# Kernel optimization log

Hardware: AMD Instinct MI355X
Metric: run time of the kernel (lower is better)

The kernel has to match this reference:

```python
import jax, jax.numpy as jnp
import numpy as np

H = 8
HID = 512
DH = HID // H
EPS = 1e-5


def _ln(x, g, b):
    mu = jnp.mean(x, axis=-1, keepdims=True)
    var = jnp.mean(jnp.square(x - mu), axis=-1, keepdims=True)
    return (x - mu) * jax.lax.rsqrt(var + EPS) * g + b


def setup_inputs() -> dict:
    key = jax.random.key(0)
    ks = jax.random.split(key, 40)
    L, M, P, D = 4096, 1024, 4096, 512

    def xav(k, shp):
        lim = np.sqrt(6.0 / (shp[0] + shp[1]))
        return jax.random.uniform(k, shp, jnp.float32, -lim, lim)

    inp = {
        'lncRNA_embedding': jax.random.normal(ks[0], (L, D), jnp.float32),
        'miRNA_embedding': jax.random.normal(ks[1], (M, D), jnp.float32),
        'protein_embedding': jax.random.normal(ks[2], (P, D), jnp.float32),
        'lncRNA_miRNA_matrix': jax.random.randint(ks[3], (L, M), 0, 2, jnp.int32),
        'protein_miRNA_matrix': jax.random.randint(ks[4], (P, M), 0, 2, jnp.int32),
    }
    names = ['Wl', 'Wm', 'Wp', 'Wql', 'Wkl', 'Wvl', 'Wqp', 'Wkp', 'Wvp']
    for i, n in enumerate(names):
        inp[n] = xav(ks[5 + i], (HID, HID))
        inp['b' + n[1:]] = jnp.zeros((HID,), jnp.float32)
    inp['Wml'] = xav(ks[20], (2 * HID, D // 2))
    inp['bml'] = jnp.zeros((D // 2,), jnp.float32)
    inp['Wmp'] = xav(ks[21], (2 * HID, D // 2))
    inp['bmp'] = jnp.zeros((D // 2,), jnp.float32)
    inp['g1'] = jnp.ones((D // 2,), jnp.float32)
    inp['be1'] = jnp.zeros((D // 2,), jnp.float32)
    inp['g2'] = jnp.ones((D // 2,), jnp.float32)
    inp['be2'] = jnp.zeros((D // 2,), jnp.float32)
    # first three linears take dim-D input (D == HID here)
    return inp


def reference(lncRNA_embedding, miRNA_embedding, protein_embedding,
              lncRNA_miRNA_matrix, protein_miRNA_matrix,
              Wl, bl, Wm, bm, Wp, bp,
              Wql, bql, Wkl, bkl, Wvl, bvl,
              Wqp, bqp, Wkp, bkp, Wvp, bvp,
              Wml, bml, Wmp, bmp, g1, be1, g2, be2):
    L = lncRNA_embedding.shape[0]
    M = miRNA_embedding.shape[0]
    P = protein_embedding.shape[0]

    lt = lncRNA_embedding @ Wl + bl          # [L, HID]
    mt = miRNA_embedding @ Wm + bm           # [M, HID]
    pt = protein_embedding @ Wp + bp         # [P, HID]

    def heads(x, W, b, n):
        return (x @ W + b).reshape(n, H, DH)

    Ql = heads(lt, Wql, bql, L)              # [L, H, DH]
    Kl = heads(mt, Wkl, bkl, M)
    Vl = heads(mt, Wvl, bvl, M)
    Qp = heads(pt, Wqp, bqp, P)
    Kp = heads(mt, Wkp, bkp, M)
    Vp = heads(mt, Wvp, bvp, M)

    scale = 1.0 / np.sqrt(DH)
    sl = jnp.einsum('lhd,mhd->hlm', Ql, Kl) * scale      # [H, L, M]
    sl = jnp.where(lncRNA_miRNA_matrix[None] == 0, -1e9, sl)
    awl = jax.nn.softmax(sl, axis=-1)

    sp = jnp.einsum('phd,mhd->hpm', Qp, Kp) * scale      # [H, P, M]
    sp = jnp.where(protein_miRNA_matrix[None] == 0, -1e9, sp)
    awp = jax.nn.softmax(sp, axis=-1)

    ctx_l = jax.nn.relu(jnp.einsum('hlm,mhd->lhd', awl, Vl).reshape(L, HID))
    ctx_p = jax.nn.relu(jnp.einsum('hpm,mhd->phd', awp, Vp).reshape(P, HID))

    mutual = jnp.einsum('hlm,hpm->lp', awl, awp) / H     # [L, P]

    fin_l = ctx_l + mutual @ ctx_p
    fin_p = ctx_p + mutual.T @ ctx_l

    out_l = _ln(jnp.concatenate([lt, fin_l], axis=-1) @ Wml + bml, g1, be1)
    out_p = _ln(jnp.concatenate([fin_p, pt], axis=-1) @ Wmp + bmp, g2, be2)
    return out_l, out_p
```

## Files before the change

kernel.cpp:

```cpp
#include <hip/hip_runtime.h>
#include <hip/hip_bf16.h>

using bf16 = __hip_bfloat16;
typedef __attribute__((ext_vector_type(8))) short short8;
typedef __attribute__((ext_vector_type(4))) float floatx4;
typedef __attribute__((ext_vector_type(8))) unsigned short ushort8;
typedef __attribute__((ext_vector_type(4))) int i32x4;
typedef __attribute__((ext_vector_type(8))) int i32x8;

__device__ __forceinline__ float b2f(unsigned short u) {
    union { unsigned int i; float f; } x; x.i = ((unsigned int)u) << 16; return x.f;
}

__device__ __forceinline__ void async16(const void* g, void* l) {
    __builtin_amdgcn_global_load_lds((const __attribute__((address_space(1))) void*)g,
                                     (__attribute__((address_space(3))) void*)l,
                                     16, 0, 0);
}

__device__ __forceinline__ unsigned char f2e4m3(float f) {
    unsigned s = (__float_as_uint(f) >> 24) & 0x80u;
    f = fminf(fabsf(f), 448.f);
    if (f < 0.015625f) {
        int d = (int)rintf(f * 512.f);
        return (unsigned char)(s | (unsigned)d);
    }
    int E = (int)((__float_as_uint(f) >> 23) & 255u) - 127;
    float ulp_inv = __uint_as_float((unsigned)(127 + 3 - E) << 23);
    int m = (int)rintf(f * ulp_inv);
    int n = (m == 16) ? ((E + 8) << 3) : (((E + 7) << 3) + (m - 8));
    if (n > 0x7E) n = 0x7E;
    return (unsigned char)(s | (unsigned)n);
}

__global__ void sniff_dtype(const unsigned short* p, int* flag) {
    int wild = 0;
    for (int i = threadIdx.x; i < 256; i += 64) {
        float a = fabsf(b2f(p[i]));
        if (!(a <= 1e4f)) wild++;
    }
#pragma unroll
    for (int o = 1; o < 64; o <<= 1) wild += __shfl_xor(wild, o);
    if (threadIdx.x == 0) *flag = (wild > 16) ? 1 : 0;
}

struct Cvt { const void* src; bf16* dst; int n; };
struct CvtTable { Cvt e[18]; };

__global__ __launch_bounds__(256) void convert_inputs(CvtTable t, const int* flag) {
    const Cvt c = t.e[blockIdx.y];
    const bool f32 = (*flag != 0);
    const int stride = gridDim.x * 256 * 8;
    for (int i = (blockIdx.x * 256 + threadIdx.x) * 8; i < c.n; i += stride) {
        if (f32) {
            const float* s = (const float*)c.src + i;
#pragma unroll
            for (int j = 0; j < 8; ++j) c.dst[i + j] = __float2bfloat16(s[j]);
        } else {
            *(ushort8*)((unsigned short*)c.dst + i) =
                *(const ushort8*)((const unsigned short*)c.src + i);
        }
    }
}

struct TT9 { const void* src[9]; bf16* dst[9]; };

__global__ __launch_bounds__(256) void transpose_sq9(TT9 t, const int* flag) {
    __shared__ bf16 tile[32][33];
    const void* in = t.src[blockIdx.z];
    bf16* out = t.dst[blockIdx.z];
    const bool f32 = (*flag != 0);
    const int tx = threadIdx.x & 31;
    const int ty = threadIdx.x >> 5;
    const int bc = blockIdx.x * 32;
    const int br = blockIdx.y * 32;
#pragma unroll
    for (int i = 0; i < 32; i += 8) {
        const size_t idx = (size_t)(br + ty + i) * 512 + bc + tx;
        tile[ty + i][tx] = f32 ? __float2bfloat16(((const float*)in)[idx])
                               : ((const bf16*)in)[idx];
    }
    __syncthreads();
#pragma unroll
    for (int i = 0; i < 32; i += 8)
        out[(size_t)(bc + ty + i) * 512 + br + tx] = tile[tx][ty + i];
}

struct TaPair { const void* in[2]; bf16* out[2]; };

__global__ __launch_bounds__(256) void transpose_any_pair(
    TaPair P, int ils, int R, int C, const int* __restrict__ flag)
{
    __shared__ bf16 tile[32][33];
    const void* in = P.in[blockIdx.z];
    bf16* out = P.out[blockIdx.z];
    const bool f32 = (*flag != 0);
    const int tx = threadIdx.x & 31;
    const int ty = threadIdx.x >> 5;
    const int bc = blockIdx.x * 32;
    const int br = blockIdx.y * 32;
#pragma unroll
    for (int i = 0; i < 32; i += 8) {
        const size_t idx = (size_t)(br + ty + i) * ils + bc + tx;
        tile[ty + i][tx] = f32 ? __float2bfloat16(((const float*)in)[idx])
                               : ((const bf16*)in)[idx];
    }
    __syncthreads();
#pragma unroll
    for (int i = 0; i < 32; i += 8)
        out[(size_t)(bc + ty + i) * R + br + tx] = tile[tx][ty + i];
}

struct TqPair { const bf16* in[2]; unsigned char* out[2]; };

__global__ __launch_bounds__(256) void transpose_q8_pair(
    TqPair P, int ils, int R, int C, float vs)
{
    __shared__ float tile[32][33];
    const bf16* in = P.in[blockIdx.z];
    unsigned char* out = P.out[blockIdx.z];
    const int tx = threadIdx.x & 31;
    const int ty = threadIdx.x >> 5;
    const int bc = blockIdx.x * 32;
    const int br = blockIdx.y * 32;
#pragma unroll
    for (int i = 0; i < 32; i += 8)
        tile[ty + i][tx] =
            __bfloat162float(in[(size_t)(br + ty + i) * ils + bc + tx]) * vs;
    __syncthreads();
#pragma unroll
    for (int i = 0; i < 32; i += 8)
        out[(size_t)(bc + ty + i) * R + br + tx] = f2e4m3(tile[tx][ty + i]);
}

__global__ __launch_bounds__(256) void transpose_b8(
    const unsigned char* __restrict__ in, unsigned char* __restrict__ out,
    int R, int C)
{
    __align__(16) __shared__ unsigned char tile[64][80];
    const int t  = threadIdx.x;
    const int r  = t & 63;
    const int cq = t >> 6;
    const int br = blockIdx.y * 64;
    const int bc = blockIdx.x * 64;
    *(i32x4*)&tile[r][cq * 16] =
        *(const i32x4*)(in + (size_t)(br + r) * C + bc + cq * 16);
    __syncthreads();
    unsigned char v[16];
#pragma unroll
    for (int j = 0; j < 16; ++j) v[j] = tile[cq * 16 + j][r];
    *(i32x4*)(out + (size_t)(bc + r) * R + br + cq * 16) = *(i32x4*)v;
}

struct BtArgs { const bf16* A; const bf16* B; void* C; const bf16* bias; };
struct BtPair { BtArgs s[2]; };

template <int BM, int BN, bool BIAS, bool F32OUT>
__global__ __launch_bounds__(256) void gemm_bt(
    BtPair P, int lda, int ldb, int ldc, int K, float scale)
{
    constexpr int WM = BM / 2;
    constexpr int WN = BN / 2;
    constexpr int TM = WM / 16;
    constexpr int TN = WN / 16;

    __align__(16) __shared__ bf16 As[BM * 64];
    __align__(16) __shared__ bf16 Bs[BN * 64];

    const BtArgs g = P.s[blockIdx.z];
    const int lane = threadIdx.x & 63;
    const int wv   = threadIdx.x >> 6;
    const int m_base = blockIdx.y * BM;
    const int n_base = blockIdx.x * BN;
    const int wm0 = (wv >> 1) * WM;
    const int wn0 = (wv & 1) * WN;

    floatx4 zero = {0.f, 0.f, 0.f, 0.f};
    floatx4 acc[TM][TN];
#pragma unroll
    for (int mt = 0; mt < TM; ++mt)
#pragma unroll
        for (int nt = 0; nt < TN; ++nt) acc[mt][nt] = zero;

    const int sr  = lane >> 3;
    const int sce = ((lane & 7) ^ sr) * 8;
    const int fr  = lane & 15;
    const int q   = lane >> 4;
    const int sw  = fr & 7;

    for (int k0 = 0; k0 < K; k0 += 64) {
#pragma unroll
        for (int cc = 0; cc < BM / 32; ++cc) {
            const int r0t = (wv + cc * 4) * 8;
            async16(g.A + (size_t)(m_base + r0t + sr) * lda + k0 + sce, &As[r0t * 64]);
        }
#pragma unroll
        for (int cc = 0; cc < BN / 32; ++cc) {
            const int r0t = (wv + cc * 4) * 8;
            async16(g.B + (size_t)(n_base + r0t + sr) * ldb + k0 + sce, &Bs[r0t * 64]);
        }
        __syncthreads();

#pragma unroll
        for (int s = 0; s < 2; ++s) {
            const int off = ((s * 4 + q) ^ sw) * 8;
            short8 af[TM], bfr[TN];
#pragma unroll
            for (int mt = 0; mt < TM; ++mt)
                af[mt] = *(const short8*)&As[(wm0 + mt * 16 + fr) * 64 + off];
#pragma unroll
            for (int nt = 0; nt < TN; ++nt)
                bfr[nt] = *(const short8*)&Bs[(wn0 + nt * 16 + fr) * 64 + off];
#pragma unroll
            for (int mt = 0; mt < TM; ++mt)
#pragma unroll
                for (int nt = 0; nt < TN; ++nt)
                    acc[mt][nt] = __builtin_amdgcn_mfma_f32_16x16x32_bf16(
                        af[mt], bfr[nt], acc[mt][nt], 0, 0, 0);
        }
        __syncthreads();
    }

    const int er = lane >> 4;
    const int ec = lane & 15;
#pragma unroll
    for (int nt = 0; nt < TN; ++nt) {
        const int col = n_base + wn0 + nt * 16 + ec;
        float bv = 0.f;
        if constexpr (BIAS) bv = __bfloat162float(g.bias[col]);
#pragma unroll
        for (int mt = 0; mt < TM; ++mt) {
#pragma unroll
            for (int r = 0; r < 4; ++r) {
                const int row = m_base + wm0 + mt * 16 + er * 4 + r;
                float v = acc[mt][nt][r] * scale + bv;
                if constexpr (F32OUT)
                    ((float*)g.C)[(size_t)row * ldc + col] = v;
                else
                    ((bf16*)g.C)[(size_t)row * ldc + col] = __float2bfloat16(v);
            }
        }
    }
}

struct SegTab { const bf16* W[3]; const bf16* bias[3]; bf16* C[3]; int ldc[3]; int rs[3]; };

__global__ __launch_bounds__(256) void gemm_bt_seg(
    const bf16* __restrict__ A, SegTab T, int K)
{
    constexpr int BM = 64, BN = 64, TM = 2, TN = 2;
    __align__(16) __shared__ bf16 As[BM * 64];
    __align__(16) __shared__ bf16 Bs[BN * 64];

    const int lane = threadIdx.x & 63;
    const int wv   = threadIdx.x >> 6;
    const int gm   = blockIdx.y * BM;
    const int seg  = (gm >= 5120) ? 2 : ((gm >= 4096) ? 1 : 0);
    const bf16* B  = T.W[seg];
    const bf16* bias = T.bias[seg];
    bf16* C        = T.C[seg];
    const int ldc  = T.ldc[seg];
    const int m_base = gm - T.rs[seg];
    const int n_base = blockIdx.x * BN;
    const int wm0 = (wv >> 1) * 32;
    const int wn0 = (wv & 1) * 32;

    floatx4 zero = {0.f, 0.f, 0.f, 0.f};
    floatx4 acc[TM][TN];
#pragma unroll
    for (int mt = 0; mt < TM; ++mt)
#pragma unroll
        for (int nt = 0; nt < TN; ++nt) acc[mt][nt] = zero;

    const int sr  = lane >> 3;
    const int sce = ((lane & 7) ^ sr) * 8;
    const int fr  = lane & 15;
    const int q   = lane >> 4;
    const int sw  = fr & 7;

    for (int k0 = 0; k0 < K; k0 += 64) {
#pragma unroll
        for (int cc = 0; cc < 2; ++cc) {
            const int r0t = (wv + cc * 4) * 8;
            async16(A + (size_t)(gm + r0t + sr) * 512 + k0 + sce, &As[r0t * 64]);
            async16(B + (size_t)(n_base + r0t + sr) * 512 + k0 + sce, &Bs[r0t * 64]);
        }
        __syncthreads();
#pragma unroll
        for (int s = 0; s < 2; ++s) {
            const int off = ((s * 4 + q) ^ sw) * 8;
            short8 af[TM], bfr[TN];
#pragma unroll
            for (int mt = 0; mt < TM; ++mt)
                af[mt] = *(const short8*)&As[(wm0 + mt * 16 + fr) * 64 + off];
#pragma unroll
            for (int nt = 0; nt < TN; ++nt)
                bfr[nt] = *(const short8*)&Bs[(wn0 + nt * 16 + fr) * 64 + off];
#pragma unroll
            for (int mt = 0; mt < TM; ++mt)
#pragma unroll
                for (int nt = 0; nt < TN; ++nt)
                    acc[mt][nt] = __builtin_amdgcn_mfma_f32_16x16x32_bf16(
                        af[mt], bfr[nt], acc[mt][nt], 0, 0, 0);
        }
        __syncthreads();
    }

    const int er = lane >> 4;
    const int ec = lane & 15;
#pragma unroll
    for (int nt = 0; nt < TN; ++nt) {
        const int col = n_base + wn0 + nt * 16 + ec;
        const float bv = __bfloat162float(bias[col]);
#pragma unroll
        for (int mt = 0; mt < TM; ++mt) {
#pragma unroll
            for (int r = 0; r < 4; ++r) {
                const int row = m_base + wm0 + mt * 16 + er * 4 + r;
                C[(size_t)row * ldc + col] =
                    __float2bfloat16(acc[mt][nt][r] + bv);
            }
        }
    }
}

struct B8Args { const unsigned char* A; const unsigned char* B; bf16* C; };
struct B8Pair { B8Args s[2]; };

template <int BM, int BN, bool RELU>
__global__ __launch_bounds__(256) void gemm_bt8(
    B8Pair P, int lda, long long a_kshift, int ldb, int ldc, int K, float scale)
{
    constexpr int WM = BM / 2;
    constexpr int WN = BN / 2;
    constexpr int TM = WM / 16;
    constexpr int TN = WN / 16;

    __align__(16) __shared__ unsigned char As[BM * 64];
    __align__(16) __shared__ unsigned char Bs[BN * 64];

    const B8Args g = P.s[blockIdx.z];
    const int lane = threadIdx.x & 63;
    const int wv   = threadIdx.x >> 6;
    const int m_base = blockIdx.y * BM;
    const int n_base = blockIdx.x * BN;
    const unsigned char* A = g.A + (long long)blockIdx.x * a_kshift;

    const int wm0 = (wv >> 1) * WM;
    const int wn0 = (wv & 1) * WN;

    floatx4 zero = {0.f, 0.f, 0.f, 0.f};
    floatx4 acc[TM][TN];
#pragma unroll
    for (int mt = 0; mt < TM; ++mt)
#pragma unroll
        for (int nt = 0; nt < TN; ++nt) acc[mt][nt] = zero;

    const int ar = lane >> 2;
    const int ac = (((lane & 3) ^ (ar & 3)) * 16);
    const int fr = lane & 15;
    const int q  = lane >> 4;
    const int sw = fr & 3;

    for (int k0 = 0; k0 < K; k0 += 64) {
#pragma unroll
        for (int cc = 0; cc < BM / 16; cc += 4) {
            const int r0t = (wv + cc) * 16;
            async16(A + (size_t)(m_base + r0t + ar) * lda + k0 + ac, &As[r0t * 64]);
        }
#pragma unroll
        for (int cc = 0; cc < BN / 16; cc += 4) {
            const int r0t = (wv + cc) * 16;
            async16(g.B + (size_t)(n_base + r0t + ar) * ldb + k0 + ac, &Bs[r0t * 64]);
        }
        __syncthreads();

#pragma unroll
        for (int s = 0; s < 2; ++s) {
            const int boff = (((s * 2 + (q >> 1)) ^ sw) * 16) + (q & 1) * 8;
            long af[TM], bfr[TN];
#pragma unroll
            for (int mt = 0; mt < TM; ++mt)
                af[mt] = *(const long*)&As[(wm0 + mt * 16 + fr) * 64 + boff];
#pragma unroll
            for (int nt = 0; nt < TN; ++nt)
                bfr[nt] = *(const long*)&Bs[(wn0 + nt * 16 + fr) * 64 + boff];
#pragma unroll
            for (int mt = 0; mt < TM; ++mt)
#pragma unroll
                for (int nt = 0; nt < TN; ++nt)
                    acc[mt][nt] = __builtin_amdgcn_mfma_f32_16x16x32_fp8_fp8(
                        af[mt], bfr[nt], acc[mt][nt], 0, 0, 0);
        }
        __syncthreads();
    }

    const int er = lane >> 4;
    const int ec = lane & 15;
#pragma unroll
    for (int nt = 0; nt < TN; ++nt) {
        const int col = n_base + wn0 + nt * 16 + ec;
#pragma unroll
        for (int mt = 0; mt < TM; ++mt) {
#pragma unroll
            for (int r = 0; r < 4; ++r) {
                const int row = m_base + wm0 + mt * 16 + er * 4 + r;
                float v = acc[mt][nt][r] * scale;
                if constexpr (RELU) v = fmaxf(v, 0.f);
                g.C[(size_t)row * ldc + col] = __float2bfloat16(v);
            }
        }
    }
}

struct MxArgs { const unsigned char* A; const unsigned char* B; void* C; const bf16* Cz; };
struct MxPair { MxArgs s[2]; };

template <int BM, int BN, bool ADDC0, bool FP8OUT>
__global__ __launch_bounds__(256) void gemm_bt8mx(
    MxPair P, int lda, int ldb, int ldc, int ldc0, int K, float scale)
{
    constexpr int WM = BM / 2;
    constexpr int WN = BN / 2;
    constexpr int TM = WM / 16;
    constexpr int TN = WN / 16;

    __align__(16) __shared__ unsigned char As[BM * 128];
    __align__(16) __shared__ unsigned char Bs[BN * 128];

    const MxArgs g = P.s[blockIdx.z];
    const int lane = threadIdx.x & 63;
    const int wv   = threadIdx.x >> 6;
    const int m_base = blockIdx.y * BM;
    const int n_base = blockIdx.x * BN;

    const int wm0 = (wv >> 1) * WM;
    const int wn0 = (wv & 1) * WN;

    floatx4 zero = {0.f, 0.f, 0.f, 0.f};
    floatx4 acc[TM][TN];
#pragma unroll
    for (int mt = 0; mt < TM; ++mt)
#pragma unroll
        for (int nt = 0; nt < TN; ++nt) acc[mt][nt] = zero;

    const int sr = lane >> 3;
    const int sc = ((lane & 7) ^ sr) * 16;
    const int fr = lane & 15;
    const int q  = lane >> 4;
    const int sw = fr & 7;

    for (int k0 = 0; k0 < K; k0 += 128) {
#pragma unroll
        for (int cc = 0; cc < BM / 32; ++cc) {
            const int r0t = (wv + cc * 4) * 8;
            async16(g.A + (size_t)(m_base + r0t + sr) * lda + k0 + sc, &As[r0t * 128]);
        }
#pragma unroll
        for (int cc = 0; cc < BN / 32; ++cc) {
            const int r0t = (wv + cc * 4) * 8;
            async16(g.B + (size_t)(n_base + r0t + sr) * ldb + k0 + sc, &Bs[r0t * 128]);
        }
        __syncthreads();

        i32x8 af[TM], bf8[TN];
#pragma unroll
        for (int mt = 0; mt < TM; ++mt) {
            const unsigned char* rp = &As[(wm0 + mt * 16 + fr) * 128];
            i32x4 lo = *(const i32x4*)(rp + (((q * 2 + 0) ^ sw) * 16));
            i32x4 hi = *(const i32x4*)(rp + (((q * 2 + 1) ^ sw) * 16));
            af[mt] = __builtin_shufflevector(lo, hi, 0, 1, 2, 3, 4, 5, 6, 7);
        }
#pragma unroll
        for (int nt = 0; nt < TN; ++nt) {
            const unsigned char* rp = &Bs[(wn0 + nt * 16 + fr) * 128];
            i32x4 lo = *(const i32x4*)(rp + (((q * 2 + 0) ^ sw) * 16));
            i32x4 hi = *(const i32x4*)(rp + (((q * 2 + 1) ^ sw) * 16));
            bf8[nt] = __builtin_shufflevector(lo, hi, 0, 1, 2, 3, 4, 5, 6, 7);
        }
#pragma unroll
        for (int mt = 0; mt < TM; ++mt)
#pragma unroll
            for (int nt = 0; nt < TN; ++nt)
                acc[mt][nt] = __builtin_amdgcn_mfma_scale_f32_16x16x128_f8f6f4(
                    af[mt], bf8[nt], acc[mt][nt],
                    0, 0, 0, 127, 0, 127);
        __syncthreads();
    }

    const int er = lane >> 4;
    const int ec = lane & 15;
#pragma unroll
    for (int nt = 0; nt < TN; ++nt) {
        const int col = n_base + wn0 + nt * 16 + ec;
#pragma unroll
        for (int mt = 0; mt < TM; ++mt) {
#pragma unroll
            for (int r = 0; r < 4; ++r) {
                const int row = m_base + wm0 + mt * 16 + er * 4 + r;
                float v = acc[mt][nt][r] * scale;
                if constexpr (ADDC0) v += __bfloat162float(g.Cz[(size_t)row * ldc0 + col]);
                if constexpr (FP8OUT)
                    ((unsigned char*)g.C)[(size_t)row * ldc + col] = f2e4m3(v);
                else
                    ((bf16*)g.C)[(size_t)row * ldc + col] = __float2bfloat16(v);
            }
        }
    }
}

struct ScArgs { const bf16* Q; const bf16* K; const int* mask; unsigned char* aw; };
struct ScPair { ScArgs s[2]; };

__global__ __launch_bounds__(256) void scores_mfma(
    ScPair P, int ldk, float scale)
{
    __shared__ float wred[16][4];
    __shared__ float wsum[16][4];

    const ScArgs g = P.s[blockIdx.z];
    const int t    = threadIdx.x;
    const int lane = t & 63;
    const int w    = t >> 6;
    const int h    = blockIdx.y;
    const int r0   = blockIdx.x * 16;
    const int fr   = lane & 15;
    const int fq   = lane >> 4;
    const int cbase = w * 256;

    const short* Qs = (const short*)g.Q + (size_t)(r0 + fr) * 512 + h * 64 + fq * 8;
    short8 a0 = *(const short8*)(Qs);
    short8 a1 = *(const short8*)(Qs + 32);

    floatx4 accs[16];
    const short* Kb = (const short*)g.K + h * 64 + fq * 8;
#pragma unroll
    for (int c = 0; c < 16; ++c) {
        const int krow = cbase + c * 16 + fr;
        short8 b0 = *(const short8*)(Kb + (size_t)krow * ldk);
        short8 b1 = *(const short8*)(Kb + (size_t)krow * ldk + 32);
        floatx4 acc = {0.f, 0.f, 0.f, 0.f};
        acc = __builtin_amdgcn_mfma_f32_16x16x32_bf16(a0, b0, acc, 0, 0, 0);
        acc = __builtin_amdgcn_mfma_f32_16x16x32_bf16(a1, b1, acc, 0, 0, 0);
        accs[c] = acc;
    }

    float mxr[4] = {-3e38f, -3e38f, -3e38f, -3e38f};
#pragma unroll
    for (int c = 0; c < 16; ++c) {
        const int col = cbase + c * 16 + fr;
#pragma unroll
        for (int r = 0; r < 4; ++r) {
            const int row = r0 + fq * 4 + r;
            float v = (g.mask[(size_t)row * 1024 + col] == 0) ? -1e9f
                                                              : accs[c][r] * scale;
            accs[c][r] = v;
            mxr[r] = fmaxf(mxr[r], v);
        }
    }
#pragma unroll
    for (int o = 1; o < 16; o <<= 1)
#pragma unroll
        for (int r = 0; r < 4; ++r) mxr[r] = fmaxf(mxr[r], __shfl_xor(mxr[r], o));
    if (fr == 0)
#pragma unroll
        for (int r = 0; r < 4; ++r) wred[fq * 4 + r][w] = mxr[r];
    __syncthreads();

    float mx[4], sm[4] = {0.f, 0.f, 0.f, 0.f};
#pragma unroll
    for (int r = 0; r < 4; ++r) {
        const int row = fq * 4 + r;
        mx[r] = fmaxf(fmaxf(wred[row][0], wred[row][1]),
                      fmaxf(wred[row][2], wred[row][3]));
    }
#pragma unroll
    for (int c = 0; c < 16; ++c)
#pragma unroll
        for (int r = 0; r < 4; ++r) {
            float e = __expf(accs[c][r] - mx[r]);
            accs[c][r] = e;
            sm[r] += e;
        }
#pragma unroll
    for (int o = 1; o < 16; o <<= 1)
#pragma unroll
        for (int r = 0; r < 4; ++r) sm[r] += __shfl_xor(sm[r], o);
    if (fr == 0)
#pragma unroll
        for (int r = 0; r < 4; ++r) wsum[fq * 4 + r][w] = sm[r];
    __syncthreads();

    float inv[4];
#pragma unroll
    for (int r = 0; r < 4; ++r) {
        const int row = fq * 4 + r;
        inv[r] = 32.0f / (wsum[row][0] + wsum[row][1] + wsum[row][2] + wsum[row][3]);
    }
#pragma unroll
    for (int c = 0; c < 16; ++c) {
        const int col = cbase + c * 16 + fr;
#pragma unroll
        for (int r = 0; r < 4; ++r) {
            const int row = r0 + fq * 4 + r;
            g.aw[(size_t)row * 8192 + h * 1024 + col] = f2e4m3(accs[c][r] * inv[r]);
        }
    }
}

__global__ __launch_bounds__(256) void ln_all(
    const float* __restrict__ X,
    const bf16* __restrict__ g1, const bf16* __restrict__ be1,
    const bf16* __restrict__ g2, const bf16* __restrict__ be2,
    void* __restrict__ out, const int* __restrict__ flag)
{
    const bool f32 = (*flag != 0);
    const int lane = threadIdx.x & 63;
    const int wv   = threadIdx.x >> 6;
    const int row  = blockIdx.x * 4 + wv;
    const bf16* gg = (row >= 4096) ? g2 : g1;
    const bf16* bb = (row >= 4096) ? be2 : be1;
    const float* x = X + (size_t)row * 256;
    float v[4], s = 0.f, s2 = 0.f;
#pragma unroll
    for (int i = 0; i < 4; ++i) {
        v[i] = x[lane + 64 * i];
        s += v[i]; s2 += v[i] * v[i];
    }
#pragma unroll
    for (int o = 1; o < 64; o <<= 1) { s += __shfl_xor(s, o); s2 += __shfl_xor(s2, o); }
    const float mu  = s * (1.0f / 256.0f);
    const float var = fmaxf(s2 * (1.0f / 256.0f) - mu * mu, 0.0f);
    const float inv = rsqrtf(var + 1e-5f);
#pragma unroll
    for (int i = 0; i < 4; ++i) {
        const int c = lane + 64 * i;
        const float y = (v[i] - mu) * inv * __bfloat162float(gg[c]) + __bfloat162float(bb[c]);
        if (f32) ((float*)out)[(size_t)row * 256 + c] = y;
        else     ((bf16*)out)[(size_t)row * 256 + c] = __float2bfloat16(y);
    }
}

extern "C" void kernel_launch(void* const* d_in, const int* in_sizes, int n_in,
                              void* d_out, int out_size, void* d_ws, size_t ws_size,
                              hipStream_t stream)
{
    const int L = 4096, Mm = 1024, P = 4096;

    const int* mask_l = (const int*)d_in[3];
    const int* mask_p = (const int*)d_in[4];

    char* ws = (char*)d_ws;
    size_t off = 0;
    auto alloc = [&](size_t bytes) {
        void* p = ws + off; off += (bytes + 255) & ~(size_t)255; return p;
    };

    int*  flag   = (int*)alloc(256);
    bf16* wt_all = (bf16*)alloc((size_t)9 * 512 * 512 * 2);
    bf16* WmlT   = (bf16*)alloc(1024 * 256 * 2);
    bf16* WmpT   = (bf16*)alloc(1024 * 256 * 2);
    bf16* b_l    = (bf16*)alloc(512 * 2);
    bf16* b_m    = (bf16*)alloc(512 * 2);
    bf16* b_p    = (bf16*)alloc(512 * 2);
    bf16* b_ql   = (bf16*)alloc(512 * 2);
    bf16* b_qp   = (bf16*)alloc(512 * 2);
    bf16* bcat   = (bf16*)alloc(2048 * 2);
    bf16* bml_c  = (bf16*)alloc(256 * 2);
    bf16* bmp_c  = (bf16*)alloc(256 * 2);
    bf16* g1c    = (bf16*)alloc(256 * 2);
    bf16* be1c   = (bf16*)alloc(256 * 2);
    bf16* g2c    = (bf16*)alloc(256 * 2);
    bf16* be2c   = (bf16*)alloc(256 * 2);
    bf16* emb_all = (bf16*)alloc((size_t)(L + Mm + P) * 512 * 2);
    bf16* embl   = emb_all;
    bf16* embm   = emb_all + (size_t)L * 512;
    bf16* embp   = embm + (size_t)Mm * 512;
    bf16* cat_l  = (bf16*)alloc((size_t)L * 1024 * 2);
    bf16* cat_p  = (bf16*)alloc((size_t)P * 1024 * 2);
    bf16* mt     = (bf16*)alloc((size_t)Mm * 512 * 2);
    bf16* Ql     = (bf16*)alloc((size_t)L * 512 * 2);
    bf16* Qp     = (bf16*)alloc((size_t)P * 512 * 2);
    bf16* kvcat  = (bf16*)alloc((size_t)Mm * 2048 * 2);
    unsigned char* V8lT = (unsigned char*)alloc((size_t)512 * Mm);
    unsigned char* V8pT = (unsigned char*)alloc((size_t)512 * Mm);
    bf16* ctx_l  = (bf16*)alloc((size_t)L * 512 * 2);
    bf16* ctx_p  = (bf16*)alloc((size_t)P * 512 * 2);
    unsigned char* ctx8lT = (unsigned char*)alloc((size_t)512 * L);
    unsigned char* ctx8pT = (unsigned char*)alloc((size_t)512 * P);
    unsigned char* mutual8 = (unsigned char*)alloc((size_t)L * P);
    unsigned char* awl8 = (unsigned char*)alloc((size_t)L * 8192);
    unsigned char* awp8 = (unsigned char*)alloc((size_t)P * 8192);
    unsigned char* mutual8T = awl8;
    float* tmp1 = (float*)awp8;

    sniff_dtype<<<1, 64, 0, stream>>>((const unsigned short*)d_in[0], flag);

    CvtTable tab;
    tab.e[0]  = { d_in[0],  embl, L * 512 };
    tab.e[1]  = { d_in[1],  embm, Mm * 512 };
    tab.e[2]  = { d_in[2],  embp, P * 512 };
    tab.e[3]  = { d_in[6],  b_l,  512 };
    tab.e[4]  = { d_in[8],  b_m,  512 };
    tab.e[5]  = { d_in[10], b_p,  512 };
    tab.e[6]  = { d_in[12], b_ql, 512 };
    tab.e[7]  = { d_in[18], b_qp, 512 };
    tab.e[8]  = { d_in[14], bcat,        512 };
    tab.e[9]  = { d_in[16], bcat + 512,  512 };
    tab.e[10] = { d_in[20], bcat + 1024, 512 };
    tab.e[11] = { d_in[22], bcat + 1536, 512 };
    tab.e[12] = { d_in[24], bml_c, 256 };
    tab.e[13] = { d_in[26], bmp_c, 256 };
    tab.e[14] = { d_in[27], g1c,  256 };
    tab.e[15] = { d_in[28], be1c, 256 };
    tab.e[16] = { d_in[29], g2c,  256 };
    tab.e[17] = { d_in[30], be2c, 256 };
    convert_inputs<<<dim3(256, 18), 256, 0, stream>>>(tab, flag);

    TT9 tt;
    const int slot_of[9] = {0, 1, 2, 3, 5, 6, 4, 7, 8};
    for (int i = 0; i < 9; ++i) {
        tt.src[i] = d_in[5 + 2 * i];
        tt.dst[i] = wt_all + (size_t)slot_of[i] * 512 * 512;
    }
    transpose_sq9<<<dim3(16, 16, 9), 256, 0, stream>>>(tt, flag);
    TaPair tw = { { d_in[23], d_in[25] }, { WmlT, WmpT } };
    transpose_any_pair<<<dim3(8, 32, 2), 256, 0, stream>>>(tw, 256, 1024, 256, flag);

    bf16* WlT  = wt_all;
    bf16* WmT  = wt_all + (size_t)1 * 512 * 512;
    bf16* WpT  = wt_all + (size_t)2 * 512 * 512;
    bf16* WqlT = wt_all + (size_t)3 * 512 * 512;
    bf16* WqpT = wt_all + (size_t)4 * 512 * 512;
    bf16* WkvT = wt_all + (size_t)5 * 512 * 512;

    SegTab st;
    st.W[0] = WlT;  st.bias[0] = b_l; st.C[0] = cat_l;       st.ldc[0] = 1024; st.rs[0] = 0;
    st.W[1] = WmT;  st.bias[1] = b_m; st.C[1] = mt;          st.ldc[1] = 512;  st.rs[1] = 4096;
    st.W[2] = WpT;  st.bias[2] = b_p; st.C[2] = cat_p + 512; st.ldc[2] = 1024; st.rs[2] = 5120;
    gemm_bt_seg<<<dim3(8, 144), 256, 0, stream>>>(emb_all, st, 512);

    BtPair qp = { { { cat_l,       WqlT, Ql, b_ql },
                    { cat_p + 512, WqpT, Qp, b_qp } } };
    gemm_bt<64, 64, true, false><<<dim3(8, 64, 2), 256, 0, stream>>>(
        qp, 1024, 512, 512, 512, 1.0f);
    BtPair kv = { { { mt, WkvT, kvcat, bcat }, { mt, WkvT, kvcat, bcat } } };
    gemm_bt<64, 64, true, false><<<dim3(32, 16, 1), 256, 0, stream>>>(
        kv, 512, 512, 2048, 512, 1.0f);

    TqPair v8 = { { kvcat + 512, kvcat + 1536 }, { V8lT, V8pT } };
    transpose_q8_pair<<<dim3(16, 32, 2), 256, 0, stream>>>(v8, 2048, 1024, 512, 4.0f);

    ScPair sc = { { { Ql, kvcat,        mask_l, awl8 },
                    { Qp, kvcat + 1024, mask_p, awp8 } } };
    scores_mfma<<<dim3(256, 8, 2), 256, 0, stream>>>(sc, 2048, 0.125f);

    B8Pair cx = { { { awl8, V8lT, ctx_l }, { awp8, V8pT, ctx_p } } };
    gemm_bt8<64, 64, true><<<dim3(8, 64, 2), 256, 0, stream>>>(
        cx, 8192, 1024, 1024, 512, 1024, 1.0f / 128.0f);

    TqPair c8 = { { ctx_l, ctx_p }, { ctx8lT, ctx8pT } };
    transpose_q8_pair<<<dim3(16, 128, 2), 256, 0, stream>>>(c8, 512, 4096, 512, 16.0f);

    MxPair mu = { { { awl8, awp8, mutual8, nullptr },
                    { awl8, awp8, mutual8, nullptr } } };
    gemm_bt8mx<128, 128, false, true><<<dim3(32, 32, 1), 256, 0, stream>>>(
        mu, 8192, 8192, 4096, 0, 8192, 0.03125f);
    transpose_b8<<<dim3(64, 64), 256, 0, stream>>>(mutual8, mutual8T, 4096, 4096);

    MxPair fn = { { { mutual8,  ctx8pT, cat_l + 512, ctx_l },
                    { mutual8T, ctx8lT, cat_p,       ctx_p } } };
    gemm_bt8mx<64, 64, true, false><<<dim3(8, 64, 2), 256, 0, stream>>>(
        fn, 4096, 4096, 1024, 512, 4096, 1.0f / 4096.0f);

    BtPair fp = { { { cat_l, WmlT, tmp1,                    bml_c },
                    { cat_p, WmpT, tmp1 + (size_t)L * 256,  bmp_c } } };
    gemm_bt<64, 64, true, true><<<dim3(4, 64, 2), 256, 0, stream>>>(
        fp, 1024, 1024, 256, 1024, 1.0f);

    ln_all<<<dim3(2048), 256, 0, stream>>>(tmp1, g1c, be1c, g2c, be2c, d_out, flag);
}
```

Measured before the change: 563.9 us.

## Fuse prep kernels, merge Q/KV GEMMs, fuse transposes into producer epilogues

Merges dtype sniffing, input conversion and weight transposes into a single prep kernel that sniffs the dtype per wave. The Q and KV projections now run in one launch. The V fp8 transpose is folded into the scores kernel, and the ctx fp8 transpose into the ctx GEMM epilogue. The mutual GEMM writes its transposed copy directly in its epilogue, uses larger tiles, and gets its own buffer instead of aliasing awl8. This is meant to cut launch count and extra memory passes, at the cost of more complex kernels and some redundant sniff work in every block.

```diff
diff --git a/kernel.cpp b/kernel.cpp
--- a/kernel.cpp
+++ b/kernel.cpp
@@ -33,213 +33,80 @@
     return (unsigned char)(s | (unsigned)n);
 }
 
-__global__ void sniff_dtype(const unsigned short* p, int* flag) {
+__device__ __forceinline__ bool sniff_wave(const unsigned short* p) {
+    const int lane = threadIdx.x & 63;
     int wild = 0;
-    for (int i = threadIdx.x; i < 256; i += 64) {
-        float a = fabsf(b2f(p[i]));
-        if (!(a <= 1e4f)) wild++;
+#pragma unroll
+    for (int j = 0; j < 4; ++j) {
+        float a = fabsf(b2f(p[lane * 4 + j]));
+        wild += !(a <= 1e4f);
     }
 #pragma unroll
     for (int o = 1; o < 64; o <<= 1) wild += __shfl_xor(wild, o);
-    if (threadIdx.x == 0) *flag = (wild > 16) ? 1 : 0;
+    return wild > 16;
 }
 
 struct Cvt { const void* src; bf16* dst; int n; };
-struct CvtTable { Cvt e[18]; };
-
-__global__ __launch_bounds__(256) void convert_inputs(CvtTable t, const int* flag) {
-    const Cvt c = t.e[blockIdx.y];
-    const bool f32 = (*flag != 0);
-    const int stride = gridDim.x * 256 * 8;
-    for (int i = (blockIdx.x * 256 + threadIdx.x) * 8; i < c.n; i += stride) {
-        if (f32) {
-            const float* s = (const float*)c.src + i;
-#pragma unroll
-            for (int j = 0; j < 8; ++j) c.dst[i + j] = __float2bfloat16(s[j]);
-        } else {
-            *(ushort8*)((unsigned short*)c.dst + i) =
-                *(const ushort8*)((const unsigned short*)c.src + i);
-        }
-    }
-}
-
-struct TT9 { const void* src[9]; bf16* dst[9]; };
-
-__global__ __launch_bounds__(256) void transpose_sq9(TT9 t, const int* flag) {
+struct PrepArgs {
+    Cvt cv[18];
+    const void* tsrc[11];
+    bf16* tdst[11];
+    const unsigned short* sn;
+};
+
+__global__ __launch_bounds__(256) void prep(PrepArgs a) {
+    const bool f32 = sniff_wave(a.sn);
+    const int y = blockIdx.y;
     __shared__ bf16 tile[32][33];
-    const void* in = t.src[blockIdx.z];
-    bf16* out = t.dst[blockIdx.z];
-    const bool f32 = (*flag != 0);
+
+    if (y < 18) {
+        const Cvt c = a.cv[y];
+        const int stride = gridDim.x * 256 * 8;
+        for (int i = (blockIdx.x * 256 + threadIdx.x) * 8; i < c.n; i += stride) {
+            if (f32) {
+                const float* s = (const float*)c.src + i;
+#pragma unroll
+                for (int j = 0; j < 8; ++j) c.dst[i + j] = __float2bfloat16(s[j]);
+            } else {
+                *(ushort8*)((unsigned short*)c.dst + i) =
+                    *(const ushort8*)((const unsigned short*)c.src + i);
+            }
+        }
+        return;
+    }
+
     const int tx = threadIdx.x & 31;
     const int ty = threadIdx.x >> 5;
-    const int bc = blockIdx.x * 32;
-    const int br = blockIdx.y * 32;
-#pragma unroll
-    for (int i = 0; i < 32; i += 8) {
-        const size_t idx = (size_t)(br + ty + i) * 512 + bc + tx;
-        tile[ty + i][tx] = f32 ? __float2bfloat16(((const float*)in)[idx])
-                               : ((const bf16*)in)[idx];
-    }
-    __syncthreads();
-#pragma unroll
-    for (int i = 0; i < 32; i += 8)
-        out[(size_t)(bc + ty + i) * 512 + br + tx] = tile[tx][ty + i];
-}
-
-struct TaPair { const void* in[2]; bf16* out[2]; };
-
-__global__ __launch_bounds__(256) void transpose_any_pair(
-    TaPair P, int ils, int R, int C, const int* __restrict__ flag)
-{
-    __shared__ bf16 tile[32][33];
-    const void* in = P.in[blockIdx.z];
-    bf16* out = P.out[blockIdx.z];
-    const bool f32 = (*flag != 0);
-    const int tx = threadIdx.x & 31;
-    const int ty = threadIdx.x >> 5;
-    const int bc = blockIdx.x * 32;
-    const int br = blockIdx.y * 32;
-#pragma unroll
-    for (int i = 0; i < 32; i += 8) {
-        const size_t idx = (size_t)(br + ty + i) * ils + bc + tx;
-        tile[ty + i][tx] = f32 ? __float2bfloat16(((const float*)in)[idx])
-                               : ((const bf16*)in)[idx];
-    }
-    __syncthreads();
-#pragma unroll
-    for (int i = 0; i < 32; i += 8)
-        out[(size_t)(bc + ty + i) * R + br + tx] = tile[tx][ty + i];
-}
-
-struct TqPair { const bf16* in[2]; unsigned char* out[2]; };
-
-__global__ __launch_bounds__(256) void transpose_q8_pair(
-    TqPair P, int ils, int R, int C, float vs)
-{
-    __shared__ float tile[32][33];
-    const bf16* in = P.in[blockIdx.z];
-    unsigned char* out = P.out[blockIdx.z];
-    const int tx = threadIdx.x & 31;
-    const int ty = threadIdx.x >> 5;
-    const int bc = blockIdx.x * 32;
-    const int br = blockIdx.y * 32;
-#pragma unroll
-    for (int i = 0; i < 32; i += 8)
-        tile[ty + i][tx] =
-            __bfloat162float(in[(size_t)(br + ty + i) * ils + bc + tx]) * vs;
-    __syncthreads();
-#pragma unroll
-    for (int i = 0; i < 32; i += 8)
-        out[(size_t)(bc + ty + i) * R + br + tx] = f2e4m3(tile[tx][ty + i]);
-}
-
-__global__ __launch_bounds__(256) void transpose_b8(
-    const unsigned char* __restrict__ in, unsigned char* __restrict__ out,
-    int R, int C)
-{
-    __align__(16) __shared__ unsigned char tile[64][80];
-    const int t  = threadIdx.x;
-    const int r  = t & 63;
-    const int cq = t >> 6;
-    const int br = blockIdx.y * 64;
-    const int bc = blockIdx.x * 64;
-    *(i32x4*)&tile[r][cq * 16] =
-        *(const i32x4*)(in + (size_t)(br + r) * C + bc + cq * 16);
-    __syncthreads();
-    unsigned char v[16];
-#pragma unroll
-    for (int j = 0; j < 16; ++j) v[j] = tile[cq * 16 + j][r];
-    *(i32x4*)(out + (size_t)(bc + r) * R + br + cq * 16) = *(i32x4*)v;
-}
-
-struct BtArgs { const bf16* A; const bf16* B; void* C; const bf16* bias; };
-struct BtPair { BtArgs s[2]; };
-
-template <int BM, int BN, bool BIAS, bool F32OUT>
-__global__ __launch_bounds__(256) void gemm_bt(
-    BtPair P, int lda, int ldb, int ldc, int K, float scale)
-{
-    constexpr int WM = BM / 2;
-    constexpr int WN = BN / 2;
-    constexpr int TM = WM / 16;
-    constexpr int TN = WN / 16;
-
-    __align__(16) __shared__ bf16 As[BM * 64];
-    __align__(16) __shared__ bf16 Bs[BN * 64];
-
-    const BtArgs g = P.s[blockIdx.z];
-    const int lane = threadIdx.x & 63;
-    const int wv   = threadIdx.x >> 6;
-    const int m_base = blockIdx.y * BM;
-    const int n_base = blockIdx.x * BN;
-    const int wm0 = (wv >> 1) * WM;
-    const int wn0 = (wv & 1) * WN;
-
-    floatx4 zero = {0.f, 0.f, 0.f, 0.f};
-    floatx4 acc[TM][TN];
-#pragma unroll
-    for (int mt = 0; mt < TM; ++mt)
-#pragma unroll
-        for (int nt = 0; nt < TN; ++nt) acc[mt][nt] = zero;
-
-    const int sr  = lane >> 3;
-    const int sce = ((lane & 7) ^ sr) * 8;
-    const int fr  = lane & 15;
-    const int q   = lane >> 4;
-    const int sw  = fr & 7;
-
-    for (int k0 = 0; k0 < K; k0 += 64) {
-#pragma unroll
-        for (int cc = 0; cc < BM / 32; ++cc) {
-            const int r0t = (wv + cc * 4) * 8;
-            async16(g.A + (size_t)(m_base + r0t + sr) * lda + k0 + sce, &As[r0t * 64]);
-        }
-#pragma unroll
-        for (int cc = 0; cc < BN / 32; ++cc) {
-            const int r0t = (wv + cc * 4) * 8;
-            async16(g.B + (size_t)(n_base + r0t + sr) * ldb + k0 + sce, &Bs[r0t * 64]);
-        }
-        __syncthreads();
-
-#pragma unroll
-        for (int s = 0; s < 2; ++s) {
-            const int off = ((s * 4 + q) ^ sw) * 8;
-            short8 af[TM], bfr[TN];
-#pragma unroll
-            for (int mt = 0; mt < TM; ++mt)
-                af[mt] = *(const short8*)&As[(wm0 + mt * 16 + fr) * 64 + off];
-#pragma unroll
-            for (int nt = 0; nt < TN; ++nt)
-                bfr[nt] = *(const short8*)&Bs[(wn0 + nt * 16 + fr) * 64 + off];
-#pragma unroll
-            for (int mt = 0; mt < TM; ++mt)
-#pragma unroll
-                for (int nt = 0; nt < TN; ++nt)
-                    acc[mt][nt] = __builtin_amdgcn_mfma_f32_16x16x32_bf16(
-                        af[mt], bfr[nt], acc[mt][nt], 0, 0, 0);
-        }
-        __syncthreads();
-    }
-
-    const int er = lane >> 4;
-    const int ec = lane & 15;
-#pragma unroll
-    for (int nt = 0; nt < TN; ++nt) {
-        const int col = n_base + wn0 + nt * 16 + ec;
-        float bv = 0.f;
-        if constexpr (BIAS) bv = __bfloat162float(g.bias[col]);
-#pragma unroll
-        for (int mt = 0; mt < TM; ++mt) {
-#pragma unroll
-            for (int r = 0; r < 4; ++r) {
-                const int row = m_base + wm0 + mt * 16 + er * 4 + r;
-                float v = acc[mt][nt][r] * scale + bv;
-                if constexpr (F32OUT)
-                    ((float*)g.C)[(size_t)row * ldc + col] = v;
-                else
-                    ((bf16*)g.C)[(size_t)row * ldc + col] = __float2bfloat16(v);
-            }
-        }
+    if (y < 27) {
+        const void* in = a.tsrc[y - 18];
+        bf16* out = a.tdst[y - 18];
+        const int bc = (blockIdx.x & 15) * 32;
+        const int br = (blockIdx.x >> 4) * 32;
+#pragma unroll
+        for (int i = 0; i < 32; i += 8) {
+            const size_t idx = (size_t)(br + ty + i) * 512 + bc + tx;
+            tile[ty + i][tx] = f32 ? __float2bfloat16(((const float*)in)[idx])
+                                   : ((const bf16*)in)[idx];
+        }
+        __syncthreads();
+#pragma unroll
+        for (int i = 0; i < 32; i += 8)
+            out[(size_t)(bc + ty + i) * 512 + br + tx] = tile[tx][ty + i];
+    } else {
+        const void* in = a.tsrc[y - 27 + 9];
+        bf16* out = a.tdst[y - 27 + 9];
+        const int bc = (blockIdx.x & 7) * 32;
+        const int br = (blockIdx.x >> 3) * 32;
+#pragma unroll
+        for (int i = 0; i < 32; i += 8) {
+            const size_t idx = (size_t)(br + ty + i) * 256 + bc + tx;
+            tile[ty + i][tx] = f32 ? __float2bfloat16(((const float*)in)[idx])
+                                   : ((const bf16*)in)[idx];
+        }
+        __syncthreads();
+#pragma unroll
+        for (int i = 0; i < 32; i += 8)
+            out[(size_t)(bc + ty + i) * 1024 + br + tx] = tile[tx][ty + i];
     }
 }
 
@@ -248,20 +115,20 @@
 __global__ __launch_bounds__(256) void gemm_bt_seg(
     const bf16* __restrict__ A, SegTab T, int K)
 {
-    constexpr int BM = 64, BN = 64, TM = 2, TN = 2;
-    __align__(16) __shared__ bf16 As[BM * 64];
-    __align__(16) __shared__ bf16 Bs[BN * 64];
+    constexpr int TM = 2, TN = 2;
+    __align__(16) __shared__ bf16 As[64 * 64];
+    __align__(16) __shared__ bf16 Bs[64 * 64];
 
     const int lane = threadIdx.x & 63;
     const int wv   = threadIdx.x >> 6;
-    const int gm   = blockIdx.y * BM;
+    const int gm   = blockIdx.y * 64;
     const int seg  = (gm >= 5120) ? 2 : ((gm >= 4096) ? 1 : 0);
     const bf16* B  = T.W[seg];
     const bf16* bias = T.bias[seg];
     bf16* C        = T.C[seg];
     const int ldc  = T.ldc[seg];
     const int m_base = gm - T.rs[seg];
-    const int n_base = blockIdx.x * BN;
+    const int n_base = blockIdx.x * 64;
     const int wm0 = (wv >> 1) * 32;
     const int wn0 = (wv & 1) * 32;
 
@@ -313,41 +180,38 @@
         const int col = n_base + wn0 + nt * 16 + ec;
         const float bv = __bfloat162float(bias[col]);
 #pragma unroll
-        for (int mt = 0; mt < TM; ++mt) {
+        for (int mt = 0; mt < TM; ++mt)
 #pragma unroll
             for (int r = 0; r < 4; ++r) {
                 const int row = m_base + wm0 + mt * 16 + er * 4 + r;
-                C[(size_t)row * ldc + col] =
-                    __float2bfloat16(acc[mt][nt][r] + bv);
+                C[(size_t)row * ldc + col] = __float2bfloat16(acc[mt][nt][r] + bv);
             }
-        }
-    }
-}
-
-struct B8Args { const unsigned char* A; const unsigned char* B; bf16* C; };
-struct B8Pair { B8Args s[2]; };
-
-template <int BM, int BN, bool RELU>
-__global__ __launch_bounds__(256) void gemm_bt8(
-    B8Pair P, int lda, long long a_kshift, int ldb, int ldc, int K, float scale)
+    }
+}
+
+struct BtArgs { const bf16* A; const bf16* B; void* C; const bf16* bias;
+                int lda, ldb, ldc; };
+struct BtSet { BtArgs s[3]; };
+
+template <bool F32OUT, bool REMAP2>
+__global__ __launch_bounds__(256) void gemm_btx(BtSet P, int K, float scale)
 {
-    constexpr int WM = BM / 2;
-    constexpr int WN = BN / 2;
-    constexpr int TM = WM / 16;
-    constexpr int TN = WN / 16;
-
-    __align__(16) __shared__ unsigned char As[BM * 64];
-    __align__(16) __shared__ unsigned char Bs[BN * 64];
-
-    const B8Args g = P.s[blockIdx.z];
+    constexpr int TM = 2, TN = 2;
+    __align__(16) __shared__ bf16 As[64 * 64];
+    __align__(16) __shared__ bf16 Bs[64 * 64];
+
+    const BtArgs g = P.s[blockIdx.z];
+    int bx = blockIdx.x, by = blockIdx.y;
+    if (REMAP2 && blockIdx.z == 2) {
+        const int flat = by * gridDim.x + bx;
+        bx = flat & 31; by = flat >> 5;
+    }
     const int lane = threadIdx.x & 63;
     const int wv   = threadIdx.x >> 6;
-    const int m_base = blockIdx.y * BM;
-    const int n_base = blockIdx.x * BN;
-    const unsigned char* A = g.A + (long long)blockIdx.x * a_kshift;
-
-    const int wm0 = (wv >> 1) * WM;
-    const int wn0 = (wv & 1) * WN;
+    const int m_base = by * 64;
+    const int n_base = bx * 64;
+    const int wm0 = (wv >> 1) * 32;
+    const int wn0 = (wv & 1) * 32;
 
     floatx4 zero = {0.f, 0.f, 0.f, 0.f};
     floatx4 acc[TM][TN];
@@ -356,40 +220,35 @@
 #pragma unroll
         for (int nt = 0; nt < TN; ++nt) acc[mt][nt] = zero;
 
-    const int ar = lane >> 2;
-    const int ac = (((lane & 3) ^ (ar & 3)) * 16);
-    const int fr = lane & 15;
-    const int q  = lane >> 4;
-    const int sw = fr & 3;
+    const int sr  = lane >> 3;
+    const int sce = ((lane & 7) ^ sr) * 8;
+    const int fr  = lane & 15;
+    const int q   = lane >> 4;
+    const int sw  = fr & 7;
 
     for (int k0 = 0; k0 < K; k0 += 64) {
 #pragma unroll
-        for (int cc = 0; cc < BM / 16; cc += 4) {
-            const int r0t = (wv + cc) * 16;
-            async16(A + (size_t)(m_base + r0t + ar) * lda + k0 + ac, &As[r0t * 64]);
-        }
-#pragma unroll
-        for (int cc = 0; cc < BN / 16; cc += 4) {
-            const int r0t = (wv + cc) * 16;
-            async16(g.B + (size_t)(n_base + r0t + ar) * ldb + k0 + ac, &Bs[r0t * 64]);
-        }
-        __syncthreads();
-
+        for (int cc = 0; cc < 2; ++cc) {
+            const int r0t = (wv + cc * 4) * 8;
+            async16(g.A + (size_t)(m_base + r0t + sr) * g.lda + k0 + sce, &As[r0t * 64]);
+            async16(g.B + (size_t)(n_base + r0t + sr) * g.ldb + k0 + sce, &Bs[r0t * 64]);
+        }
+        __syncthreads();
 #pragma unroll
         for (int s = 0; s < 2; ++s) {
-            const int boff = (((s * 2 + (q >> 1)) ^ sw) * 16) + (q & 1) * 8;
-            long af[TM], bfr[TN];
+            const int off = ((s * 4 + q) ^ sw) * 8;
+            short8 af[TM], bfr[TN];
 #pragma unroll
             for (int mt = 0; mt < TM; ++mt)
-                af[mt] = *(const long*)&As[(wm0 + mt * 16 + fr) * 64 + boff];
+                af[mt] = *(const short8*)&As[(wm0 + mt * 16 + fr) * 64 + off];
 #pragma unroll
             for (int nt = 0; nt < TN; ++nt)
-                bfr[nt] = *(const long*)&Bs[(wn0 + nt * 16 + fr) * 64 + boff];
+                bfr[nt] = *(const short8*)&Bs[(wn0 + nt * 16 + fr) * 64 + off];
 #pragma unroll
             for (int mt = 0; mt < TM; ++mt)
 #pragma unroll
                 for (int nt = 0; nt < TN; ++nt)
-                    acc[mt][nt] = __builtin_amdgcn_mfma_f32_16x16x32_fp8_fp8(
+                    acc[mt][nt] = __builtin_amdgcn_mfma_f32_16x16x32_bf16(
                         af[mt], bfr[nt], acc[mt][nt], 0, 0, 0);
         }
         __syncthreads();
@@ -400,123 +259,51 @@
 #pragma unroll
     for (int nt = 0; nt < TN; ++nt) {
         const int col = n_base + wn0 + nt * 16 + ec;
-#pragma unroll
-        for (int mt = 0; mt < TM; ++mt) {
+        const float bv = __bfloat162float(g.bias[col]);
+#pragma unroll
+        for (int mt = 0; mt < TM; ++mt)
 #pragma unroll
             for (int r = 0; r < 4; ++r) {
                 const int row = m_base + wm0 + mt * 16 + er * 4 + r;
-                float v = acc[mt][nt][r] * scale;
-                if constexpr (RELU) v = fmaxf(v, 0.f);
-                g.C[(size_t)row * ldc + col] = __float2bfloat16(v);
+                const float v = acc[mt][nt][r] * scale + bv;
+                if constexpr (F32OUT)
+                    ((float*)g.C)[(size_t)row * g.ldc + col] = v;
+                else
+                    ((bf16*)g.C)[(size_t)row * g.ldc + col] = __float2bfloat16(v);
             }
-        }
-    }
-}
-
-struct MxArgs { const unsigned char* A; const unsigned char* B; void* C; const bf16* Cz; };
-struct MxPair { MxArgs s[2]; };
-
-template <int BM, int BN, bool ADDC0, bool FP8OUT>
-__global__ __launch_bounds__(256) void gemm_bt8mx(
-    MxPair P, int lda, int ldb, int ldc, int ldc0, int K, float scale)
-{
-    constexpr int WM = BM / 2;
-    constexpr int WN = BN / 2;
-    constexpr int TM = WM / 16;
-    constexpr int TN = WN / 16;
-
-    __align__(16) __shared__ unsigned char As[BM * 128];
-    __align__(16) __shared__ unsigned char Bs[BN * 128];
-
-    const MxArgs g = P.s[blockIdx.z];
-    const int lane = threadIdx.x & 63;
-    const int wv   = threadIdx.x >> 6;
-    const int m_base = blockIdx.y * BM;
-    const int n_base = blockIdx.x * BN;
-
-    const int wm0 = (wv >> 1) * WM;
-    const int wn0 = (wv & 1) * WN;
-
-    floatx4 zero = {0.f, 0.f, 0.f, 0.f};
-    floatx4 acc[TM][TN];
-#pragma unroll
-    for (int mt = 0; mt < TM; ++mt)
-#pragma unroll
-        for (int nt = 0; nt < TN; ++nt) acc[mt][nt] = zero;
-
-    const int sr = lane >> 3;
-    const int sc = ((lane & 7) ^ sr) * 16;
-    const int fr = lane & 15;
-    const int q  = lane >> 4;
-    const int sw = fr & 7;
-
-    for (int k0 = 0; k0 < K; k0 += 128) {
-#pragma unroll
-        for (int cc = 0; cc < BM / 32; ++cc) {
-            const int r0t = (wv + cc * 4) * 8;
-            async16(g.A + (size_t)(m_base + r0t + sr) * lda + k0 + sc, &As[r0t * 128]);
-        }
-#pragma unroll
-        for (int cc = 0; cc < BN / 32; ++cc) {
-            const int r0t = (wv + cc * 4) * 8;
-            async16(g.B + (size_t)(n_base + r0t + sr) * ldb + k0 + sc, &Bs[r0t * 128]);
-        }
-        __syncthreads();
-
-        i32x8 af[TM], bf8[TN];
-#pragma unroll
-        for (int mt = 0; mt < TM; ++mt) {
-            const unsigned char* rp = &As[(wm0 + mt * 16 + fr) * 128];
-            i32x4 lo = *(const i32x4*)(rp + (((q * 2 + 0) ^ sw) * 16));
-            i32x4 hi = *(const i32x4*)(rp + (((q * 2 + 1) ^ sw) * 16));
-            af[mt] = __builtin_shufflevector(lo, hi, 0, 1, 2, 3, 4, 5, 6, 7);
-        }
-#pragma unroll
-        for (int nt = 0; nt < TN; ++nt) {
-            const unsigned char* rp = &Bs[(wn0 + nt * 16 + fr) * 128];
-            i32x4 lo = *(const i32x4*)(rp + (((q * 2 + 0) ^ sw) * 16));
-            i32x4 hi = *(const i32x4*)(rp + (((q * 2 + 1) ^ sw) * 16));
-            bf8[nt] = __builtin_shufflevector(lo, hi, 0, 1, 2, 3, 4, 5, 6, 7);
-        }
-#pragma unroll
-        for (int mt = 0; mt < TM; ++mt)
-#pragma unroll
-            for (int nt = 0; nt < TN; ++nt)
-                acc[mt][nt] = __builtin_amdgcn_mfma_scale_f32_16x16x128_f8f6f4(
-                    af[mt], bf8[nt], acc[mt][nt],
-                    0, 0, 0, 127, 0, 127);
-        __syncthreads();
-    }
-
-    const int er = lane >> 4;
-    const int ec = lane & 15;
-#pragma unroll
-    for (int nt = 0; nt < TN; ++nt) {
-        const int col = n_base + wn0 + nt * 16 + ec;
-#pragma unroll
-        for (int mt = 0; mt < TM; ++mt) {
-#pragma unroll
-            for (int r = 0; r < 4; ++r) {
-                const int row = m_base + wm0 + mt * 16 + er * 4 + r;
-                float v = acc[mt][nt][r] * scale;
-                if constexpr (ADDC0) v += __bfloat162float(g.Cz[(size_t)row * ldc0 + col]);
-                if constexpr (FP8OUT)
-                    ((unsigned char*)g.C)[(size_t)row * ldc + col] = f2e4m3(v);
-                else
-                    ((bf16*)g.C)[(size_t)row * ldc + col] = __float2bfloat16(v);
-            }
-        }
     }
 }
 
 struct ScArgs { const bf16* Q; const bf16* K; const int* mask; unsigned char* aw; };
-struct ScPair { ScArgs s[2]; };
-
-__global__ __launch_bounds__(256) void scores_mfma(
-    ScPair P, int ldk, float scale)
+struct ScSet { ScArgs s[2]; const bf16* vsrc[2]; unsigned char* vdst[2]; };
+
+__global__ __launch_bounds__(256) void scores_v8(ScSet P, int ldk, float scale)
 {
     __shared__ float wred[16][4];
     __shared__ float wsum[16][4];
+    __shared__ float tile[32][33];
+
+    if (blockIdx.z == 2) {
+        const int flat = blockIdx.y * 256 + blockIdx.x;
+        if (flat >= 1024) return;
+        const int side = flat >> 9;
+        const int rem  = flat & 511;
+        const bf16* in = P.vsrc[side];
+        unsigned char* out = P.vdst[side];
+        const int bc = (rem & 15) * 32;
+        const int br = (rem >> 4) * 32;
+        const int tx = threadIdx.x & 31;
+        const int ty = threadIdx.x >> 5;
+#pragma unroll
+        for (int i = 0; i < 32; i += 8)
+            tile[ty + i][tx] =
+                __bfloat162float(in[(size_t)(br + ty + i) * 2048 + bc + tx]) * 4.0f;
+        __syncthreads();
+#pragma unroll
+        for (int i = 0; i < 32; i += 8)
+            out[(size_t)(bc + ty + i) * 1024 + br + tx] = f2e4m3(tile[tx][ty + i]);
+        return;
+    }
 
     const ScArgs g = P.s[blockIdx.z];
     const int t    = threadIdx.x;
@@ -608,13 +395,193 @@
     }
 }
 
+struct B8Args { const unsigned char* A; const unsigned char* B; bf16* C;
+                unsigned char* CT; };
+struct B8Pair { B8Args s[2]; };
+
+__global__ __launch_bounds__(256) void gemm_bt8_ctx(
+    B8Pair P, int lda, long long a_kshift, int ldb, int ldc, int ldct,
+    int K, float scale)
+{
+    constexpr int TM = 2, TN = 2;
+    __align__(16) __shared__ unsigned char As[64 * 64];
+    __align__(16) __shared__ unsigned char Bs[64 * 64];
+
+    const B8Args g = P.s[blockIdx.z];
+    const int lane = threadIdx.x & 63;
+    const int wv   = threadIdx.x >> 6;
+    const int m_base = blockIdx.y * 64;
+    const int n_base = blockIdx.x * 64;
+    const unsigned char* A = g.A + (long long)blockIdx.x * a_kshift;
+
+    const int wm0 = (wv >> 1) * 32;
+    const int wn0 = (wv & 1) * 32;
+
+    floatx4 zero = {0.f, 0.f, 0.f, 0.f};
+    floatx4 acc[TM][TN];
+#pragma unroll
+    for (int mt = 0; mt < TM; ++mt)
+#pragma unroll
+        for (int nt = 0; nt < TN; ++nt) acc[mt][nt] = zero;
+
+    const int ar = lane >> 2;
+    const int ac = (((lane & 3) ^ (ar & 3)) * 16);
+    const int fr = lane & 15;
+    const int q  = lane >> 4;
+    const int sw = fr & 3;
+
+    for (int k0 = 0; k0 < K; k0 += 64) {
+        async16(A + (size_t)(m_base + wv * 16 + ar) * lda + k0 + ac, &As[wv * 16 * 64]);
+        async16(g.B + (size_t)(n_base + wv * 16 + ar) * ldb + k0 + ac, &Bs[wv * 16 * 64]);
+        __syncthreads();
+#pragma unroll
+        for (int s = 0; s < 2; ++s) {
+            const int boff = (((s * 2 + (q >> 1)) ^ sw) * 16) + (q & 1) * 8;
+            long af[TM], bfr[TN];
+#pragma unroll
+            for (int mt = 0; mt < TM; ++mt)
+                af[mt] = *(const long*)&As[(wm0 + mt * 16 + fr) * 64 + boff];
+#pragma unroll
+            for (int nt = 0; nt < TN; ++nt)
+                bfr[nt] = *(const long*)&Bs[(wn0 + nt * 16 + fr) * 64 + boff];
+#pragma unroll
+            for (int mt = 0; mt < TM; ++mt)
+#pragma unroll
+                for (int nt = 0; nt < TN; ++nt)
+                    acc[mt][nt] = __builtin_amdgcn_mfma_f32_16x16x32_fp8_fp8(
+                        af[mt], bfr[nt], acc[mt][nt], 0, 0, 0);
+        }
+        __syncthreads();
+    }
+
+    const int er = lane >> 4;
+    const int ec = lane & 15;
+#pragma unroll
+    for (int nt = 0; nt < TN; ++nt) {
+        const int col = n_base + wn0 + nt * 16 + ec;
+#pragma unroll
+        for (int mt = 0; mt < TM; ++mt) {
+            const int rowb = m_base + wm0 + mt * 16 + er * 4;
+            unsigned int pk = 0;
+#pragma unroll
+            for (int r = 0; r < 4; ++r) {
+                float v = fmaxf(acc[mt][nt][r] * scale, 0.f);
+                g.C[(size_t)(rowb + r) * ldc + col] = __float2bfloat16(v);
+                pk |= (unsigned)f2e4m3(v * 16.0f) << (8 * r);
+            }
+            *(unsigned int*)(g.CT + (size_t)col * ldct + rowb) = pk;
+        }
+    }
+}
+
+struct MxArgs { const unsigned char* A; const unsigned char* B; void* C;
+                const bf16* Cz; unsigned char* CT; };
+struct MxPair { MxArgs s[2]; };
+
+template <int BM, int BN, bool ADDC0, bool FP8OUT, bool TOUT>
+__global__ __launch_bounds__(256, 2) void gemm_bt8mx(
+    MxPair P, int lda, int ldb, int ldc, int ldc0, int ldct, int K, float scale)
+{
+    constexpr int WM = BM / 2;
+    constexpr int WN = BN / 2;
+    constexpr int TM = WM / 16;
+    constexpr int TN = WN / 16;
+
+    __align__(16) __shared__ unsigned char As[BM * 128];
+    __align__(16) __shared__ unsigned char Bs[BN * 128];
+
+    const MxArgs g = P.s[blockIdx.z];
+    const int lane = threadIdx.x & 63;
+    const int wv   = threadIdx.x >> 6;
+    const int m_base = blockIdx.y * BM;
+    const int n_base = blockIdx.x * BN;
+
+    const int wm0 = (wv >> 1) * WM;
+    const int wn0 = (wv & 1) * WN;
+
+    floatx4 zero = {0.f, 0.f, 0.f, 0.f};
+    floatx4 acc[TM][TN];
+#pragma unroll
+    for (int mt = 0; mt < TM; ++mt)
+#pragma unroll
+        for (int nt = 0; nt < TN; ++nt) acc[mt][nt] = zero;
+
+    const int sr = lane >> 3;
+    const int sc = ((lane & 7) ^ sr) * 16;
+    const int fr = lane & 15;
+    const int q  = lane >> 4;
+    const int sw = fr & 7;
+
+    for (int k0 = 0; k0 < K; k0 += 128) {
+#pragma unroll
+        for (int cc = 0; cc < BM / 32; ++cc) {
+            const int r0t = (wv + cc * 4) * 8;
+            async16(g.A + (size_t)(m_base + r0t + sr) * lda + k0 + sc, &As[r0t * 128]);
+        }
+#pragma unroll
+        for (int cc = 0; cc < BN / 32; ++cc) {
+            const int r0t = (wv + cc * 4) * 8;
+            async16(g.B + (size_t)(n_base + r0t + sr) * ldb + k0 + sc, &Bs[r0t * 128]);
+        }
+        __syncthreads();
+
+        i32x8 af[TM];
+#pragma unroll
+        for (int mt = 0; mt < TM; ++mt) {
+            const unsigned char* rp = &As[(wm0 + mt * 16 + fr) * 128];
+            i32x4 lo = *(const i32x4*)(rp + (((q * 2 + 0) ^ sw) * 16));
+            i32x4 hi = *(const i32x4*)(rp + (((q * 2 + 1) ^ sw) * 16));
+            af[mt] = __builtin_shufflevector(lo, hi, 0, 1, 2, 3, 4, 5, 6, 7);
+        }
+#pragma unroll
+        for (int nt = 0; nt < TN; ++nt) {
+            const unsigned char* rp = &Bs[(wn0 + nt * 16 + fr) * 128];
+            i32x4 lo = *(const i32x4*)(rp + (((q * 2 + 0) ^ sw) * 16));
+            i32x4 hi = *(const i32x4*)(rp + (((q * 2 + 1) ^ sw) * 16));
+            i32x8 bf8 = __builtin_shufflevector(lo, hi, 0, 1, 2, 3, 4, 5, 6, 7);
+#pragma unroll
+            for (int mt = 0; mt < TM; ++mt)
+                acc[mt][nt] = __builtin_amdgcn_mfma_scale_f32_16x16x128_f8f6f4(
+                    af[mt], bf8, acc[mt][nt], 0, 0, 0, 127, 0, 127);
+        }
+        __syncthreads();
+    }
+
+    const int er = lane >> 4;
+    const int ec = lane & 15;
+#pragma unroll
+    for (int nt = 0; nt < TN; ++nt) {
+        const int col = n_base + wn0 + nt * 16 + ec;
+#pragma unroll
+        for (int mt = 0; mt < TM; ++mt) {
+            const int rowb = m_base + wm0 + mt * 16 + er * 4;
+            unsigned int pk = 0;
+#pragma unroll
+            for (int r = 0; r < 4; ++r) {
+                float v = acc[mt][nt][r] * scale;
+                if constexpr (ADDC0)
+                    v += __bfloat162float(g.Cz[(size_t)(rowb + r) * ldc0 + col]);
+                if constexpr (FP8OUT) {
+                    const unsigned char qv = f2e4m3(v);
+                    ((unsigned char*)g.C)[(size_t)(rowb + r) * ldc + col] = qv;
+                    if constexpr (TOUT) pk |= (unsigned)qv << (8 * r);
+                } else {
+                    ((bf16*)g.C)[(size_t)(rowb + r) * ldc + col] = __float2bfloat16(v);
+                }
+            }
+            if constexpr (TOUT)
+                *(unsigned int*)(g.CT + (size_t)col * ldct + rowb) = pk;
+        }
+    }
+}
+
 __global__ __launch_bounds__(256) void ln_all(
     const float* __restrict__ X,
     const bf16* __restrict__ g1, const bf16* __restrict__ be1,
     const bf16* __restrict__ g2, const bf16* __restrict__ be2,
-    void* __restrict__ out, const int* __restrict__ flag)
+    void* __restrict__ out, const unsigned short* __restrict__ sn)
 {
-    const bool f32 = (*flag != 0);
+    const bool f32 = sniff_wave(sn);
     const int lane = threadIdx.x & 63;
     const int wv   = threadIdx.x >> 6;
     const int row  = blockIdx.x * 4 + wv;
@@ -649,6 +616,7 @@
 
     const int* mask_l = (const int*)d_in[3];
     const int* mask_p = (const int*)d_in[4];
+    const unsigned short* sn = (const unsigned short*)d_in[0];
 
     char* ws = (char*)d_ws;
     size_t off = 0;
@@ -656,7 +624,6 @@
         void* p = ws + off; off += (bytes + 255) & ~(size_t)255; return p;
     };
 
-    int*  flag   = (int*)alloc(256);
     bf16* wt_all = (bf16*)alloc((size_t)9 * 512 * 512 * 2);
     bf16* WmlT   = (bf16*)alloc(1024 * 256 * 2);
     bf16* WmpT   = (bf16*)alloc(1024 * 256 * 2);
@@ -688,44 +655,40 @@
     bf16* ctx_p  = (bf16*)alloc((size_t)P * 512 * 2);
     unsigned char* ctx8lT = (unsigned char*)alloc((size_t)512 * L);
     unsigned char* ctx8pT = (unsigned char*)alloc((size_t)512 * P);
-    unsigned char* mutual8 = (unsigned char*)alloc((size_t)L * P);
+    unsigned char* mutual8  = (unsigned char*)alloc((size_t)L * P);
+    unsigned char* mutual8T = (unsigned char*)alloc((size_t)L * P);
     unsigned char* awl8 = (unsigned char*)alloc((size_t)L * 8192);
     unsigned char* awp8 = (unsigned char*)alloc((size_t)P * 8192);
-    unsigned char* mutual8T = awl8;
     float* tmp1 = (float*)awp8;
 
-    sniff_dtype<<<1, 64, 0, stream>>>((const unsigned short*)d_in[0], flag);
-
-    CvtTable tab;
-    tab.e[0]  = { d_in[0],  embl, L * 512 };
-    tab.e[1]  = { d_in[1],  embm, Mm * 512 };
-    tab.e[2]  = { d_in[2],  embp, P * 512 };
-    tab.e[3]  = { d_in[6],  b_l,  512 };
-    tab.e[4]  = { d_in[8],  b_m,  512 };
-    tab.e[5]  = { d_in[10], b_p,  512 };
-    tab.e[6]  = { d_in[12], b_ql, 512 };
-    tab.e[7]  = { d_in[18], b_qp, 512 };
-    tab.e[8]  = { d_in[14], bcat,        512 };
-    tab.e[9]  = { d_in[16], bcat + 512,  512 };
-    tab.e[10] = { d_in[20], bcat + 1024, 512 };
-    tab.e[11] = { d_in[22], bcat + 1536, 512 };
-    tab.e[12] = { d_in[24], bml_c, 256 };
-    tab.e[13] = { d_in[26], bmp_c, 256 };
-    tab.e[14] = { d_in[27], g1c,  256 };
-    tab.e[15] = { d_in[28], be1c, 256 };
-    tab.e[16] = { d_in[29], g2c,  256 };
-    tab.e[17] = { d_in[30], be2c, 256 };
-    convert_inputs<<<dim3(256, 18), 256, 0, stream>>>(tab, flag);
-
-    TT9 tt;
+    PrepArgs pa;
+    pa.sn = sn;
+    pa.cv[0]  = { d_in[0],  embl, L * 512 };
+    pa.cv[1]  = { d_in[1],  embm, Mm * 512 };
+    pa.cv[2]  = { d_in[2],  embp, P * 512 };
+    pa.cv[3]  = { d_in[6],  b_l,  512 };
+    pa.cv[4]  = { d_in[8],  b_m,  512 };
+    pa.cv[5]  = { d_in[10], b_p,  512 };
+    pa.cv[6]  = { d_in[12], b_ql, 512 };
+    pa.cv[7]  = { d_in[18], b_qp, 512 };
+    pa.cv[8]  = { d_in[14], bcat,        512 };
+    pa.cv[9]  = { d_in[16], bcat + 512,  512 };
+    pa.cv[10] = { d_in[20], bcat + 1024, 512 };
+    pa.cv[11] = { d_in[22], bcat + 1536, 512 };
+    pa.cv[12] = { d_in[24], bml_c, 256 };
+    pa.cv[13] = { d_in[26], bmp_c, 256 };
+    pa.cv[14] = { d_in[27], g1c,  256 };
+    pa.cv[15] = { d_in[28], be1c, 256 };
+    pa.cv[16] = { d_in[29], g2c,  256 };
+    pa.cv[17] = { d_in[30], be2c, 256 };
     const int slot_of[9] = {0, 1, 2, 3, 5, 6, 4, 7, 8};
     for (int i = 0; i < 9; ++i) {
-        tt.src[i] = d_in[5 + 2 * i];
-        tt.dst[i] = wt_all + (size_t)slot_of[i] * 512 * 512;
-    }
-    transpose_sq9<<<dim3(16, 16, 9), 256, 0, stream>>>(tt, flag);
-    TaPair tw = { { d_in[23], d_in[25] }, { WmlT, WmpT } };
-    transpose_any_pair<<<dim3(8, 32, 2), 256, 0, stream>>>(tw, 256, 1024, 256, flag);
+        pa.tsrc[i] = d_in[5 + 2 * i];
+        pa.tdst[i] = wt_all + (size_t)slot_of[i] * 512 * 512;
+    }
+    pa.tsrc[9]  = d_in[23]; pa.tdst[9]  = WmlT;
+    pa.tsrc[10] = d_in[25]; pa.tdst[10] = WmpT;
+    prep<<<dim3(256, 29), 256, 0, stream>>>(pa);
 
     bf16* WlT  = wt_all;
     bf16* WmT  = wt_all + (size_t)1 * 512 * 512;
@@ -740,43 +703,39 @@
     st.W[2] = WpT;  st.bias[2] = b_p; st.C[2] = cat_p + 512; st.ldc[2] = 1024; st.rs[2] = 5120;
     gemm_bt_seg<<<dim3(8, 144), 256, 0, stream>>>(emb_all, st, 512);
 
-    BtPair qp = { { { cat_l,       WqlT, Ql, b_ql },
-                    { cat_p + 512, WqpT, Qp, b_qp } } };
-    gemm_bt<64, 64, true, false><<<dim3(8, 64, 2), 256, 0, stream>>>(
-        qp, 1024, 512, 512, 512, 1.0f);
-    BtPair kv = { { { mt, WkvT, kvcat, bcat }, { mt, WkvT, kvcat, bcat } } };
-    gemm_bt<64, 64, true, false><<<dim3(32, 16, 1), 256, 0, stream>>>(
-        kv, 512, 512, 2048, 512, 1.0f);
-
-    TqPair v8 = { { kvcat + 512, kvcat + 1536 }, { V8lT, V8pT } };
-    transpose_q8_pair<<<dim3(16, 32, 2), 256, 0, stream>>>(v8, 2048, 1024, 512, 4.0f);
-
-    ScPair sc = { { { Ql, kvcat,        mask_l, awl8 },
-                    { Qp, kvcat + 1024, mask_p, awp8 } } };
-    scores_mfma<<<dim3(256, 8, 2), 256, 0, stream>>>(sc, 2048, 0.125f);
-
-    B8Pair cx = { { { awl8, V8lT, ctx_l }, { awp8, V8pT, ctx_p } } };
-    gemm_bt8<64, 64, true><<<dim3(8, 64, 2), 256, 0, stream>>>(
-        cx, 8192, 1024, 1024, 512, 1024, 1.0f / 128.0f);
-
-    TqPair c8 = { { ctx_l, ctx_p }, { ctx8lT, ctx8pT } };
-    transpose_q8_pair<<<dim3(16, 128, 2), 256, 0, stream>>>(c8, 512, 4096, 512, 16.0f);
-
-    MxPair mu = { { { awl8, awp8, mutual8, nullptr },
-                    { awl8, awp8, mutual8, nullptr } } };
-    gemm_bt8mx<128, 128, false, true><<<dim3(32, 32, 1), 256, 0, stream>>>(
-        mu, 8192, 8192, 4096, 0, 8192, 0.03125f);
-    transpose_b8<<<dim3(64, 64), 256, 0, stream>>>(mutual8, mutual8T, 4096, 4096);
-
-    MxPair fn = { { { mutual8,  ctx8pT, cat_l + 512, ctx_l },
-                    { mutual8T, ctx8lT, cat_p,       ctx_p } } };
-    gemm_bt8mx<64, 64, true, false><<<dim3(8, 64, 2), 256, 0, stream>>>(
-        fn, 4096, 4096, 1024, 512, 4096, 1.0f / 4096.0f);
-
-    BtPair fp = { { { cat_l, WmlT, tmp1,                    bml_c },
-                    { cat_p, WmpT, tmp1 + (size_t)L * 256,  bmp_c } } };
-    gemm_bt<64, 64, true, true><<<dim3(4, 64, 2), 256, 0, stream>>>(
-        fp, 1024, 1024, 256, 1024, 1.0f);
-
-    ln_all<<<dim3(2048), 256, 0, stream>>>(tmp1, g1c, be1c, g2c, be2c, d_out, flag);
-}
+    BtSet qs;
+    qs.s[0] = { cat_l,       WqlT, Ql,    b_ql, 1024, 512, 512 };
+    qs.s[1] = { cat_p + 512, WqpT, Qp,    b_qp, 1024, 512, 512 };
+    qs.s[2] = { mt,          WkvT, kvcat, bcat, 512,  512, 2048 };
+    gemm_btx<false, true><<<dim3(8, 64, 3), 256, 0, stream>>>(qs, 512, 1.0f);
+
+    ScSet sc;
+    sc.s[0] = { Ql, kvcat,        mask_l, awl8 };
+    sc.s[1] = { Qp, kvcat + 1024, mask_p, awp8 };
+    sc.vsrc[0] = kvcat + 512;  sc.vdst[0] = V8lT;
+    sc.vsrc[1] = kvcat + 1536; sc.vdst[1] = V8pT;
+    scores_v8<<<dim3(256, 8, 3), 256, 0, stream>>>(sc, 2048, 0.125f);
+
+    B8Pair cx = { { { awl8, V8lT, ctx_l, ctx8lT },
+                    { awp8, V8pT, ctx_p, ctx8pT } } };
+    gemm_bt8_ctx<<<dim3(8, 64, 2), 256, 0, stream>>>(
+        cx, 8192, 1024, 1024, 512, 4096, 1024, 1.0f / 128.0f);
+
+    MxPair mu = { { { awl8, awp8, mutual8, nullptr, mutual8T },
+                    { awl8, awp8, mutual8, nullptr, mutual8T } } };
+    gemm_bt8mx<256, 128, false, true, true><<<dim3(32, 16, 1), 256, 0, stream>>>(
+        mu, 8192, 8192, 4096, 0, 4096, 8192, 0.03125f);
+
+    MxPair fn = { { { mutual8,  ctx8pT, cat_l + 512, ctx_l, nullptr },
+                    { mutual8T, ctx8lT, cat_p,       ctx_p, nullptr } } };
+    gemm_bt8mx<64, 128, true, false, false><<<dim3(4, 64, 2), 256, 0, stream>>>(
+        fn, 4096, 4096, 1024, 512, 0, 4096, 1.0f / 4096.0f);
+
+    BtSet fp;
+    fp.s[0] = { cat_l, WmlT, tmp1,                   bml_c, 1024, 1024, 256 };
+    fp.s[1] = { cat_p, WmpT, tmp1 + (size_t)L * 256, bmp_c, 1024, 1024, 256 };
+    fp.s[2] = fp.s[0];
+    gemm_btx<true, false><<<dim3(4, 64, 2), 256, 0, stream>>>(fp, 1024, 1.0f);
+
+    ln_all<<<dim3(2048), 256, 0, stream>>>(tmp1, g1c, be1c, g2c, be2c, d_out, sn);
+}
```

Result: faster. 500.0 us (-11.3%).
